# Optimization experiments

Hardware: AMD Instinct MI355X
Metric: run time of the kernel (lower is better)

Reference implementation:

```python
import jax, jax.numpy as jnp
import numpy as np

B, T, F, H, C = 512, 512, 128, 32, 6

def setup_inputs() -> dict:
    key = jax.random.key(0)
    ks = jax.random.split(key, 6)
    x = jax.random.normal(ks[0], (B, T, F), jnp.float32)
    # random valid lengths; zero-padded tails get masked by Masking(mask_value=0.0)
    lengths = jax.random.randint(ks[1], (B,), T // 4, T + 1)
    tmask = (jnp.arange(T)[None, :] < lengths[:, None]).astype(jnp.float32)
    x = x * tmask[:, :, None]
    Wx = jax.random.normal(ks[2], (F, 4 * H), jnp.float32) / np.sqrt(F).astype(np.float32)
    Wh = jax.random.normal(ks[3], (H, 4 * H), jnp.float32) / np.sqrt(H).astype(np.float32)
    b = jnp.zeros((4 * H,), jnp.float32)
    Wfc = jax.random.normal(ks[4], (H, C), jnp.float32) / np.sqrt(H).astype(np.float32)
    bfc = jnp.zeros((C,), jnp.float32)
    return dict(x=x, Wx=Wx, Wh=Wh, b=b, Wfc=Wfc, bfc=bfc)

def reference(x, Wx, Wh, b, Wfc, bfc):
    # Masking(0.0): timestep masked iff all features == 0
    mask = jnp.any(x != 0.0, axis=-1)                       # [B, T]
    Hh = Wh.shape[0]
    Bn = x.shape[0]
    xt = jnp.transpose(x, (1, 0, 2))                        # [T, B, F]
    mt = jnp.transpose(mask, (1, 0))[:, :, None].astype(x.dtype)  # [T, B, 1]
    # precompute input projection for all steps (one big GEMM)
    xz = jnp.einsum('tbf,fk->tbk', xt, Wx) + b              # [T, B, 4H]

    def step(carry, inp):
        h, c = carry
        zx, m = inp
        z = zx + h @ Wh                                     # [B, 4H]
        i, f, g, o = jnp.split(z, 4, axis=-1)               # keras gate order i,f,c,o
        i = jax.nn.sigmoid(i)
        f = jax.nn.sigmoid(f)
        g = jnp.tanh(g)
        o = jax.nn.sigmoid(o)
        c_new = f * c + i * g
        h_new = o * jnp.tanh(c_new)
        # masked steps keep previous state (Keras masked LSTM semantics)
        h = m * h_new + (1.0 - m) * h
        c = m * c_new + (1.0 - m) * c
        return (h, c), None

    h0 = jnp.zeros((Bn, Hh), x.dtype)
    (h, _), _ = jax.lax.scan(step, (h0, h0), (xz, mt))
    return jax.nn.softmax(h @ Wfc + bfc, axis=-1)           # [B, C]
```

## Files before the change

kernel.cpp:

```cpp
#include <hip/hip_runtime.h>

#define B_ 512
#define T_ 512
#define F_ 128
#define H_ 32
#define C_ 6

typedef float f32x2 __attribute__((ext_vector_type(2)));

__global__ __launch_bounds__(256, 2) void k_xz(
    const float* __restrict__ x, const float* __restrict__ W,
    const float* __restrict__ bias, float* __restrict__ xz,
    float* __restrict__ mask)
{
  __shared__ float xl[128 * 64];
  __shared__ float wl[64 * 128];
  const int tid = threadIdx.x;
  const int m0  = blockIdx.x * 128;
  const int cg  = tid & 15;
  const int rg  = tid >> 4;

  float4 xpre[8], wpre[8];
  int rowbits = 0;

  auto load_chunk = [&](int ch) {
#pragma unroll
    for (int k = 0; k < 8; ++k) {
      const int u = tid + k * 256, r = u >> 4, q = u & 15;
      xpre[k] = *(const float4*)(x + (size_t)(m0 + r) * 128 + ch * 64 + q * 4);
    }
#pragma unroll
    for (int k = 0; k < 8; ++k) {
      const int u = tid + k * 256, f = u >> 5, q = u & 31;
      wpre[k] = *(const float4*)(W + (size_t)(ch * 64 + f) * 128 + q * 4);
    }
  };
  auto mask_chunk = [&]() {
#pragma unroll
    for (int k = 0; k < 8; ++k) {
      const float4 v = xpre[k];
      int nb = ((v.x != 0.f) || (v.y != 0.f) || (v.z != 0.f) || (v.w != 0.f)) ? 1 : 0;
      nb |= __shfl_xor(nb, 1); nb |= __shfl_xor(nb, 2);
      nb |= __shfl_xor(nb, 4); nb |= __shfl_xor(nb, 8);
      rowbits |= nb << k;
    }
  };
  auto write_chunk = [&]() {
#pragma unroll
    for (int k = 0; k < 8; ++k) {
      const int u = tid + k * 256, r = u >> 4, q = u & 15;
      *(float4*)(xl + r * 64 + ((q * 4) ^ (((r >> 3) & 3) << 2))) = xpre[k];
    }
#pragma unroll
    for (int k = 0; k < 8; ++k) {
      const int u = tid + k * 256, f = u >> 5, q = u & 31;
      *(float4*)(wl + f * 128 + q * 4) = wpre[k];
    }
  };

  float acc[8][8];
#pragma unroll
  for (int r = 0; r < 8; ++r)
#pragma unroll
    for (int u = 0; u < 8; ++u) acc[r][u] = 0.f;

  auto compute = [&]() {
#pragma unroll 2
    for (int fq = 0; fq < 16; ++fq) {
      float4 xv[8];
#pragma unroll
      for (int r = 0; r < 8; ++r)
        xv[r] = *(const float4*)(xl + (rg * 8 + r) * 64 + ((fq * 4) ^ ((rg & 3) << 2)));
#pragma unroll
      for (int ff = 0; ff < 4; ++ff) {
        const float* wr = wl + (fq * 4 + ff) * 128 + cg * 4;
        const float4 wa = *(const float4*)(wr);
        const float4 wb = *(const float4*)(wr + 64);
#pragma unroll
        for (int r = 0; r < 8; ++r) {
          const float xs = (ff == 0) ? xv[r].x : (ff == 1) ? xv[r].y
                         : (ff == 2) ? xv[r].z : xv[r].w;
          acc[r][0] += xs * wa.x;  acc[r][1] += xs * wa.y;
          acc[r][2] += xs * wa.z;  acc[r][3] += xs * wa.w;
          acc[r][4] += xs * wb.x;  acc[r][5] += xs * wb.y;
          acc[r][6] += xs * wb.z;  acc[r][7] += xs * wb.w;
        }
      }
    }
  };

  load_chunk(0);
  mask_chunk();
  write_chunk();
  __syncthreads();
  load_chunk(1);
  compute();
  __syncthreads();
  mask_chunk();
  write_chunk();
  __syncthreads();
  compute();

  float bb[8];
#pragma unroll
  for (int u = 0; u < 4; ++u) {
    bb[u]     = bias[cg * 4 + u];
    bb[4 + u] = bias[64 + cg * 4 + u];
  }
#pragma unroll
  for (int r = 0; r < 8; ++r) {
    float* op = xz + (size_t)(m0 + rg * 8 + r) * 128;
    float4 o0 = { acc[r][0] + bb[0], acc[r][1] + bb[1], acc[r][2] + bb[2], acc[r][3] + bb[3] };
    float4 o1 = { acc[r][4] + bb[4], acc[r][5] + bb[5], acc[r][6] + bb[6], acc[r][7] + bb[7] };
    *(float4*)(op + cg * 4)      = o0;
    *(float4*)(op + 64 + cg * 4) = o1;
  }
  if ((tid & 15) == 0) {
#pragma unroll
    for (int k = 0; k < 8; ++k)
      mask[m0 + k * 16 + rg] = (rowbits >> k) & 1 ? 1.f : 0.f;
  }
}

__device__ __forceinline__ float sigmf(float xx) {
  return __builtin_amdgcn_rcpf(1.f + __expf(-xx));
}
__device__ __forceinline__ float tanhf_(float xx) {
  return __builtin_amdgcn_rcpf(1.f + __expf(-2.f * xx)) * 2.f - 1.f;
}

__global__ __launch_bounds__(64, 1) void k_lstm(
    const float* __restrict__ xz, const float* __restrict__ mask,
    const float* __restrict__ Wh, const float* __restrict__ Wfc,
    const float* __restrict__ bfc, float* __restrict__ out)
{
  const int lane = threadIdx.x;
  const int half = lane >> 5;
  const int j = lane & 31;
  const int b = blockIdx.x * 2 + half;

  f32x2 Whr[16][4];
#pragma unroll
  for (int q = 0; q < 16; ++q)
#pragma unroll
    for (int g = 0; g < 4; ++g) {
      Whr[q][g][0] = Wh[(2 * q)     * 128 + g * 32 + j];
      Whr[q][g][1] = Wh[(2 * q + 1) * 128 + g * 32 + j];
    }

  f32x2 hr2[16];
#pragma unroll
  for (int q = 0; q < 16; ++q) { hr2[q][0] = 0.f; hr2[q][1] = 0.f; }
  float cj = 0.f, hj = 0.f;

  __shared__ __align__(16) float hs[2][32];

  const float* xp = xz + (size_t)b * (T_ * 128) + j;
  const float* mp = mask + (size_t)b * T_;

  float xgr[4][4];
  float mr[4];
#pragma unroll
  for (int s = 0; s < 4; ++s) {
#pragma unroll
    for (int g = 0; g < 4; ++g) xgr[s][g] = xp[s * 128 + g * 32];
    mr[s] = mp[s];
  }

  for (int t0 = 0; t0 < T_; t0 += 4) {
#pragma unroll
    for (int s = 0; s < 4; ++s) {
      const int t = t0 + s;
      f32x2 a[4];
#pragma unroll
      for (int g = 0; g < 4; ++g) { a[g][0] = xgr[s][g]; a[g][1] = 0.f; }
      const float m = mr[s];

      int pf = t + 4;
      if (pf > T_ - 1) pf = T_ - 1;
#pragma unroll
      for (int g = 0; g < 4; ++g) xgr[s][g] = xp[(size_t)pf * 128 + g * 32];
      mr[s] = mp[pf];

#pragma unroll
      for (int q = 0; q < 16; ++q) {
#pragma unroll
        for (int g = 0; g < 4; ++g)
          a[g] += hr2[q] * Whr[q][g];
      }
      const float zi = a[0][0] + a[0][1];
      const float zf = a[1][0] + a[1][1];
      const float zg = a[2][0] + a[2][1];
      const float zo = a[3][0] + a[3][1];

      const float ig = sigmf(zi);
      const float fg = sigmf(zf);
      const float gg = tanhf_(zg);
      const float og = sigmf(zo);
      const float cn = fg * cj + ig * gg;
      const float hn = og * tanhf_(cn);
      cj += m * (cn - cj);
      hj += m * (hn - hj);

      hs[half][j] = hj;
      __builtin_amdgcn_wave_barrier();
#pragma unroll
      for (int q = 0; q < 8; ++q) {
        const float4 v = *(const float4*)(&hs[half][q * 4]);
        hr2[2 * q][0]     = v.x; hr2[2 * q][1]     = v.y;
        hr2[2 * q + 1][0] = v.z; hr2[2 * q + 1][1] = v.w;
      }
      __builtin_amdgcn_wave_barrier();
    }
  }

  float hrs[32];
#pragma unroll
  for (int q = 0; q < 16; ++q) { hrs[2 * q] = hr2[q][0]; hrs[2 * q + 1] = hr2[q][1]; }
  float logits[C_];
#pragma unroll
  for (int c = 0; c < C_; ++c) {
    float aa = bfc[c];
#pragma unroll
    for (int f = 0; f < 32; ++f) aa += hrs[f] * Wfc[f * C_ + c];
    logits[c] = aa;
  }
  if (j == 0) {
    float mx = logits[0];
#pragma unroll
    for (int c = 1; c < C_; ++c) mx = fmaxf(mx, logits[c]);
    float e[C_], s = 0.f;
#pragma unroll
    for (int c = 0; c < C_; ++c) { e[c] = __expf(logits[c] - mx); s += e[c]; }
    const float rs = 1.f / s;
#pragma unroll
    for (int c = 0; c < C_; ++c) out[(size_t)b * C_ + c] = e[c] * rs;
  }
}

extern "C" void kernel_launch(void* const* d_in, const int* in_sizes, int n_in,
                              void* d_out, int out_size, void* d_ws, size_t ws_size,
                              hipStream_t stream) {
  const float* x   = (const float*)d_in[0];
  const float* Wx  = (const float*)d_in[1];
  const float* Wh  = (const float*)d_in[2];
  const float* bv  = (const float*)d_in[3];
  const float* Wfc = (const float*)d_in[4];
  const float* bfc = (const float*)d_in[5];
  float* out = (float*)d_out;

  float* xz   = (float*)d_ws;
  float* mask = (float*)((char*)d_ws + (size_t)B_ * T_ * 128 * 4);

  k_xz<<<(B_ * T_) / 128, 256, 0, stream>>>(x, Wx, bv, xz, mask);
  k_lstm<<<B_ / 2, 64, 0, stream>>>(xz, mask, Wh, Wfc, bfc, out);
}
```

Measured before the change: 268.4 us.

## Stream LSTM gate inputs into LDS via async global_load_lds double buffering

The recurrent kernel now copies the precomputed input projections for chunks of 8 timesteps directly from global memory into a double-buffered LDS area, using global_load_lds with explicit vmcnt waits. This replaces the per-step register prefetch that ran only 4 steps ahead. The per-row mask is also loaded once into LDS at kernel start. The aim is to keep global load latency off the serial recurrence chain and to relieve register pressure. In exchange, each step adds LDS reads and the code relies on hand-written waitcnt ordering.

```diff
diff --git a/kernel.cpp b/kernel.cpp
--- a/kernel.cpp
+++ b/kernel.cpp
@@ -5,8 +5,12 @@
 #define F_ 128
 #define H_ 32
 #define C_ 6
+#define CH 8
+#define NCH (T_ / CH)
 
 typedef float f32x2 __attribute__((ext_vector_type(2)));
+#define AS3(p) ((__attribute__((address_space(3))) void*)(p))
+#define AS1(p) ((const __attribute__((address_space(1))) void*)(p))
 
 __global__ __launch_bounds__(256, 2) void k_xz(
     const float* __restrict__ x, const float* __restrict__ W,
@@ -134,10 +138,23 @@
     const float* __restrict__ Wh, const float* __restrict__ Wfc,
     const float* __restrict__ bfc, float* __restrict__ out)
 {
+  __shared__ float xch[2][CH][4][64];
+  __shared__ float mld[2 * T_];
+  __shared__ __align__(16) float hs[2][32];
+
   const int lane = threadIdx.x;
   const int half = lane >> 5;
-  const int j = lane & 31;
-  const int b = blockIdx.x * 2 + half;
+  const int j    = lane & 31;
+  const int b    = blockIdx.x * 2 + half;
+
+  {
+    const float* mrow = mask + (size_t)(blockIdx.x * 2) * T_;
+    float mv[16];
+#pragma unroll
+    for (int c = 0; c < 16; ++c) mv[c] = mrow[c * 64 + lane];
+#pragma unroll
+    for (int c = 0; c < 16; ++c) mld[c * 64 + lane] = mv[c];
+  }
 
   f32x2 Whr[16][4];
 #pragma unroll
@@ -153,45 +170,51 @@
   for (int q = 0; q < 16; ++q) { hr2[q][0] = 0.f; hr2[q][1] = 0.f; }
   float cj = 0.f, hj = 0.f;
 
-  __shared__ __align__(16) float hs[2][32];
-
   const float* xp = xz + (size_t)b * (T_ * 128) + j;
-  const float* mp = mask + (size_t)b * T_;
-
-  float xgr[4][4];
-  float mr[4];
-#pragma unroll
-  for (int s = 0; s < 4; ++s) {
-#pragma unroll
-    for (int g = 0; g < 4; ++g) xgr[s][g] = xp[s * 128 + g * 32];
-    mr[s] = mp[s];
-  }
-
-  for (int t0 = 0; t0 < T_; t0 += 4) {
-#pragma unroll
-    for (int s = 0; s < 4; ++s) {
-      const int t = t0 + s;
-      f32x2 a[4];
-#pragma unroll
-      for (int g = 0; g < 4; ++g) { a[g][0] = xgr[s][g]; a[g][1] = 0.f; }
-      const float m = mr[s];
-
-      int pf = t + 4;
-      if (pf > T_ - 1) pf = T_ - 1;
-#pragma unroll
-      for (int g = 0; g < 4; ++g) xgr[s][g] = xp[(size_t)pf * 128 + g * 32];
-      mr[s] = mp[pf];
-
+
+  auto issue_chunk = [&](int k, int slot) {
+#pragma unroll
+    for (int s = 0; s < CH; ++s) {
+      const float* st = xp + (size_t)(k * CH + s) * 128;
+#pragma unroll
+      for (int g = 0; g < 4; ++g)
+        __builtin_amdgcn_global_load_lds(AS1(st + g * 32),
+                                         AS3(&xch[slot][s][g][0]), 4, 0, 0);
+    }
+  };
+
+  issue_chunk(0, 0);
+
+  for (int k = 0; k < NCH; ++k) {
+    const int slot = k & 1;
+    if (k + 1 < NCH) {
+      issue_chunk(k + 1, slot ^ 1);
+      asm volatile("s_waitcnt vmcnt(32)" ::: "memory");
+    } else {
+      asm volatile("s_waitcnt vmcnt(0)" ::: "memory");
+    }
+    __builtin_amdgcn_sched_barrier(0);
+
+#pragma unroll
+    for (int s = 0; s < CH; ++s) {
+      const float xg0 = xch[slot][s][0][lane];
+      const float xg1 = xch[slot][s][1][lane];
+      const float xg2 = xch[slot][s][2][lane];
+      const float xg3 = xch[slot][s][3][lane];
+      const float m   = mld[half * T_ + k * CH + s];
+
+      f32x2 a0 = {0.f, 0.f}, a1 = {0.f, 0.f}, a2 = {0.f, 0.f}, a3 = {0.f, 0.f};
 #pragma unroll
       for (int q = 0; q < 16; ++q) {
-#pragma unroll
-        for (int g = 0; g < 4; ++g)
-          a[g] += hr2[q] * Whr[q][g];
+        a0 += hr2[q] * Whr[q][0];
+        a1 += hr2[q] * Whr[q][1];
+        a2 += hr2[q] * Whr[q][2];
+        a3 += hr2[q] * Whr[q][3];
       }
-      const float zi = a[0][0] + a[0][1];
-      const float zf = a[1][0] + a[1][1];
-      const float zg = a[2][0] + a[2][1];
-      const float zo = a[3][0] + a[3][1];
+      const float zi = xg0 + a0[0] + a0[1];
+      const float zf = xg1 + a1[0] + a1[1];
+      const float zg = xg2 + a2[0] + a2[1];
+      const float zo = xg3 + a3[0] + a3[1];
 
       const float ig = sigmf(zi);
       const float fg = sigmf(zf);
@@ -229,10 +252,10 @@
     float mx = logits[0];
 #pragma unroll
     for (int c = 1; c < C_; ++c) mx = fmaxf(mx, logits[c]);
-    float e[C_], s = 0.f;
-#pragma unroll
-    for (int c = 0; c < C_; ++c) { e[c] = __expf(logits[c] - mx); s += e[c]; }
-    const float rs = 1.f / s;
+    float e[C_], sden = 0.f;
+#pragma unroll
+    for (int c = 0; c < C_; ++c) { e[c] = __expf(logits[c] - mx); sden += e[c]; }
+    const float rs = 1.f / sden;
 #pragma unroll
     for (int c = 0; c < C_; ++c) out[(size_t)b * C_ + c] = e[c] * rs;
   }
```

After: 283.9 us. 5.8% more time.
